# Performance work log

Hardware: AMD Instinct MI355X
Metric: run time of the kernel (lower is better)

The kernel has to match this reference:

```python
import jax, jax.numpy as jnp
import numpy as np

B, L, D_MODEL = 2, 2048, 1024
D_INNER, D_STATE, D_CONV, DT_RANK = 2048, 16, 4, 64  # expand=2, dt_rank=ceil(1024/16)


def setup_inputs() -> dict:
    key = jax.random.key(0)
    ks = jax.random.split(key, 12)
    s = lambda k, shape, sc=0.02: jax.random.normal(k, shape, dtype=jnp.float32) * sc
    return {
        "x": jax.random.normal(ks[0], (B, L, D_MODEL), dtype=jnp.float32),
        "norm_w": jnp.ones((D_MODEL,), jnp.float32),
        "norm_b": jnp.zeros((D_MODEL,), jnp.float32),
        "in_proj_w": s(ks[1], (2 * D_INNER, D_MODEL)),
        "conv_w": s(ks[2], (D_INNER, 1, D_CONV), 0.1),
        "conv_b": s(ks[3], (D_INNER,), 0.1),
        "x_proj_w": s(ks[4], (DT_RANK + 2 * D_STATE, D_INNER)),
        "dt_proj_w": s(ks[5], (D_INNER, DT_RANK), 0.1),
        "dt_proj_b": s(ks[6], (D_INNER,), 0.5),
        "A_log": jnp.log(jnp.broadcast_to(jnp.arange(1, D_STATE + 1, dtype=jnp.float32), (D_INNER, D_STATE))),
        "D": jnp.ones((D_INNER,), jnp.float32),
        "out_proj_w": s(ks[7], (D_MODEL, D_INNER)),
    }


def _layernorm(x, w, b, eps=1e-5):
    mu = jnp.mean(x, axis=-1, keepdims=True)
    var = jnp.var(x, axis=-1, keepdims=True)
    return (x - mu) * jax.lax.rsqrt(var + eps) * w + b


def _mamba_forward(x, norm_w, norm_b, in_proj_w, conv_w, conv_b, x_proj_w,
                   dt_proj_w, dt_proj_b, A_log, D, out_proj_w):
    residual = x
    xn = _layernorm(x, norm_w, norm_b)
    # in_proj -> split into x-branch and gate z
    xz = jnp.einsum('bld,ed->ble', xn, in_proj_w)  # [B,L,2*D_INNER]
    xc, z = jnp.split(xz, 2, axis=-1)
    # causal depthwise conv1d over time
    xt = jnp.transpose(xc, (0, 2, 1))  # [B,C,L]
    xt = jnp.pad(xt, ((0, 0), (0, 0), (D_CONV - 1, 0)))
    xt = jax.lax.conv_general_dilated(
        xt, conv_w, window_strides=(1,), padding=[(0, 0)],
        feature_group_count=D_INNER,
        dimension_numbers=('NCH', 'OIH', 'NCH')) + conv_b[None, :, None]
    u = jax.nn.silu(jnp.transpose(xt, (0, 2, 1)))  # [B,L,D_INNER]
    # input-dependent dt, B, C
    x_dbl = jnp.einsum('bld,ed->ble', u, x_proj_w)
    dt, Bm, Cm = jnp.split(x_dbl, [DT_RANK, DT_RANK + D_STATE], axis=-1)
    dt = jax.nn.softplus(jnp.einsum('blr,dr->bld', dt, dt_proj_w) + dt_proj_b)  # [B,L,D_INNER]
    A = -jnp.exp(A_log)  # [D_INNER, D_STATE]

    def step(h, inp):
        dt_t, B_t, C_t, u_t = inp  # [B,Di],[B,Ds],[B,Ds],[B,Di]
        dA = jnp.exp(dt_t[..., None] * A)                       # [B,Di,Ds]
        h = dA * h + (dt_t * u_t)[..., None] * B_t[:, None, :]  # [B,Di,Ds]
        y_t = jnp.einsum('bds,bs->bd', h, C_t)
        return h, y_t

    xs = (jnp.transpose(dt, (1, 0, 2)), jnp.transpose(Bm, (1, 0, 2)),
          jnp.transpose(Cm, (1, 0, 2)), jnp.transpose(u, (1, 0, 2)))
    h0 = jnp.zeros((B, D_INNER, D_STATE), dtype=x.dtype)
    _, ys = jax.lax.scan(step, h0, xs)
    y = jnp.transpose(ys, (1, 0, 2)) + u * D  # [B,L,D_INNER]
    y = y * jax.nn.silu(z)
    out = jnp.einsum('ble,de->bld', y, out_proj_w)
    # dropout in eval mode = identity
    return residual + out


def reference(x, norm_w, norm_b, in_proj_w, conv_w, conv_b, x_proj_w,
              dt_proj_w, dt_proj_b, A_log, D, out_proj_w):
    return _mamba_forward(x, norm_w, norm_b, in_proj_w, conv_w, conv_b, x_proj_w,
                          dt_proj_w, dt_proj_b, A_log, D, out_proj_w)
```

## Files before the change

### kernel.cpp

```cpp
#include <hip/hip_runtime.h>
#include <hip/hip_bf16.h>
#include <math.h>

#define BB 2
#define LL 2048
#define DMODEL 1024
#define DINNER 2048
#define DSTATE 16
#define DTRANK 64
#define NROWS (BB * LL)
#define NC 32
#define CK 64
#define KS 16
#define KCH (DINNER / KS)

typedef __bf16 bf16x8 __attribute__((ext_vector_type(8)));
typedef float  f32x4  __attribute__((ext_vector_type(4)));
typedef __attribute__((address_space(3))) void       as3_void;
typedef const __attribute__((address_space(1))) void as1_cvoid;

__device__ __forceinline__ ushort f2bf(float x) {
    __hip_bfloat16 h = __float2bfloat16(x);
    return *(ushort*)&h;
}

__global__ __launch_bounds__(256) void ln_kernel(const float* __restrict__ x,
                                                 const float* __restrict__ w,
                                                 const float* __restrict__ b,
                                                 __hip_bfloat16* __restrict__ xn) {
    int row = blockIdx.x;
    const float* xr = x + (size_t)row * DMODEL;
    float4 v = reinterpret_cast<const float4*>(xr)[threadIdx.x];
    float s  = v.x + v.y + v.z + v.w;
    float ss = v.x * v.x + v.y * v.y + v.z * v.z + v.w * v.w;
    for (int off = 32; off > 0; off >>= 1) {
        s  += __shfl_down(s, off);
        ss += __shfl_down(ss, off);
    }
    __shared__ float red0[4], red1[4];
    __shared__ float mu_s, rstd_s;
    int lane = threadIdx.x & 63, wv = threadIdx.x >> 6;
    if (lane == 0) { red0[wv] = s; red1[wv] = ss; }
    __syncthreads();
    if (threadIdx.x == 0) {
        float S = red0[0] + red0[1] + red0[2] + red0[3];
        float SS = red1[0] + red1[1] + red1[2] + red1[3];
        float mu = S * (1.0f / DMODEL);
        float var = SS * (1.0f / DMODEL) - mu * mu;
        mu_s = mu;
        rstd_s = rsqrtf(var + 1e-5f);
    }
    __syncthreads();
    float mu = mu_s, rstd = rstd_s;
    float4 wv4 = reinterpret_cast<const float4*>(w)[threadIdx.x];
    float4 bv4 = reinterpret_cast<const float4*>(b)[threadIdx.x];
    ushort4 o;
    o.x = f2bf((v.x - mu) * rstd * wv4.x + bv4.x);
    o.y = f2bf((v.y - mu) * rstd * wv4.y + bv4.y);
    o.z = f2bf((v.z - mu) * rstd * wv4.z + bv4.z);
    o.w = f2bf((v.w - mu) * rstd * wv4.w + bv4.w);
    *reinterpret_cast<ushort4*>((ushort*)xn + (size_t)row * DMODEL + threadIdx.x * 4) = o;
}

__global__ __launch_bounds__(256) void cvt_kernel(const float* __restrict__ in,
                                                  __hip_bfloat16* __restrict__ o) {
    int i = (blockIdx.x * 256 + threadIdx.x) * 4;
    float4 v = *reinterpret_cast<const float4*>(in + i);
    ushort4 p;
    p.x = f2bf(v.x); p.y = f2bf(v.y); p.z = f2bf(v.z); p.w = f2bf(v.w);
    *reinterpret_cast<ushort4*>((ushort*)o + i) = p;
}

template <int EPI>
__global__ __launch_bounds__(256) void gemm_bf16(
    const __hip_bfloat16* __restrict__ A, int lda,
    const __hip_bfloat16* __restrict__ W, int ldw,
    float* __restrict__ C, float* __restrict__ C2, int nsplit, int ldc,
    int K, const float* __restrict__ R) {
    __shared__ ushort As[128][32];
    __shared__ ushort Bs[128][32];
    int tid = threadIdx.x;
    int w = tid >> 6, lane = tid & 63;
    int m0 = blockIdx.y * 128, n0 = blockIdx.x * 128;
    int wr = w >> 1, wc = w & 1;

    int srow = (w << 4) + (lane >> 2);
    int skoff = (lane & 3) << 3;
    const ushort* gA = (const ushort*)A + (size_t)(m0 + srow) * lda + skoff;
    const ushort* gB = (const ushort*)W + (size_t)(n0 + srow) * ldw + skoff;
    char* ldsA0 = (char*)&As[0][0] + w * 1024;
    char* ldsB0 = (char*)&Bs[0][0] + w * 1024;

    f32x4 acc[4][4] = {};
    int frow = (lane & 15);
    int fk   = (lane >> 4) << 3;

    for (int k0 = 0; k0 < K; k0 += 32) {
        __syncthreads();
        __builtin_amdgcn_global_load_lds((as1_cvoid*)(gA + k0),                    (as3_void*)(ldsA0),        16, 0, 0);
        __builtin_amdgcn_global_load_lds((as1_cvoid*)(gA + (size_t)64 * lda + k0), (as3_void*)(ldsA0 + 4096), 16, 0, 0);
        __builtin_amdgcn_global_load_lds((as1_cvoid*)(gB + k0),                    (as3_void*)(ldsB0),        16, 0, 0);
        __builtin_amdgcn_global_load_lds((as1_cvoid*)(gB + (size_t)64 * ldw + k0), (as3_void*)(ldsB0 + 4096), 16, 0, 0);
        __syncthreads();

        bf16x8 af[4], bfr[4];
#pragma unroll
        for (int mi = 0; mi < 4; mi++)
            af[mi] = *(const bf16x8*)&As[wr * 64 + mi * 16 + frow][fk];
#pragma unroll
        for (int ni = 0; ni < 4; ni++)
            bfr[ni] = *(const bf16x8*)&Bs[wc * 64 + ni * 16 + frow][fk];
#pragma unroll
        for (int mi = 0; mi < 4; mi++)
#pragma unroll
            for (int ni = 0; ni < 4; ni++)
                acc[mi][ni] = __builtin_amdgcn_mfma_f32_16x16x32_bf16(
                    af[mi], bfr[ni], acc[mi][ni], 0, 0, 0);
    }

    int crow = (lane >> 4) << 2;
    int ccol = lane & 15;
    float* Cb = C;
    int nbase = n0;
    if (EPI == 0 && n0 >= nsplit) { Cb = C2; nbase = n0 - nsplit; }
#pragma unroll
    for (int mi = 0; mi < 4; mi++) {
#pragma unroll
        for (int ni = 0; ni < 4; ni++) {
#pragma unroll
            for (int r = 0; r < 4; r++) {
                int m = m0 + wr * 64 + mi * 16 + crow + r;
                int n = nbase + wc * 64 + ni * 16 + ccol;
                float v = acc[mi][ni][r];
                if (EPI == 2) v += R[(size_t)m * ldc + n];
                Cb[(size_t)m * ldc + n] = v;
            }
        }
    }
}

template <int EPI>
__global__ __launch_bounds__(256) void gemm_kernel(
    const float* __restrict__ A, int lda,
    const float* __restrict__ W, int ldw,
    float* __restrict__ C, int ldc,
    int N, int K,
    const float* __restrict__ bias) {
    __shared__ float As[16][64];
    __shared__ float Ws[16][64];
    int m0 = blockIdx.y * 64;
    int n0 = blockIdx.x * 64;
    int tid = threadIdx.x;
    int tm = tid >> 4, tn = tid & 15;
    int lr = tid >> 2;
    int lk = (tid & 3) << 2;

    float acc[4][4] = {};

    for (int k0 = 0; k0 < K; k0 += 16) {
        float4 av = *reinterpret_cast<const float4*>(A + (size_t)(m0 + lr) * lda + k0 + lk);
        float4 wvv;
        int wn = n0 + lr;
        if (wn < N)
            wvv = *reinterpret_cast<const float4*>(W + (size_t)wn * ldw + k0 + lk);
        else
            wvv = make_float4(0.f, 0.f, 0.f, 0.f);
        __syncthreads();
        As[lk + 0][lr] = av.x; As[lk + 1][lr] = av.y;
        As[lk + 2][lr] = av.z; As[lk + 3][lr] = av.w;
        Ws[lk + 0][lr] = wvv.x; Ws[lk + 1][lr] = wvv.y;
        Ws[lk + 2][lr] = wvv.z; Ws[lk + 3][lr] = wvv.w;
        __syncthreads();
#pragma unroll
        for (int k = 0; k < 16; k++) {
            float4 a = *reinterpret_cast<const float4*>(&As[k][tm << 2]);
            float4 bv = *reinterpret_cast<const float4*>(&Ws[k][tn << 2]);
            float ar[4] = {a.x, a.y, a.z, a.w};
            float br[4] = {bv.x, bv.y, bv.z, bv.w};
#pragma unroll
            for (int i = 0; i < 4; i++)
#pragma unroll
                for (int j = 0; j < 4; j++)
                    acc[i][j] = fmaf(ar[i], br[j], acc[i][j]);
        }
    }
#pragma unroll
    for (int i = 0; i < 4; i++) {
        int m = m0 + (tm << 2) + i;
#pragma unroll
        for (int j = 0; j < 4; j++) {
            int n = n0 + (tn << 2) + j;
            if (n < N) {
                float v = acc[i][j];
                if (EPI == 1) {
                    v += bias[n];
                    v = (v > 20.f) ? v : log1pf(__expf(v));
                }
                C[(size_t)m * ldc + n] = v;
            }
        }
    }
}

__global__ __launch_bounds__(256) void xp_partial(
    const float* __restrict__ A,
    const float* __restrict__ W,
    float* __restrict__ P) {
    __shared__ float As[16][64];
    __shared__ float Ws[16][64];
    int m0 = blockIdx.y * 64;
    int n0 = blockIdx.x * 64;
    int kbase = blockIdx.z * KCH;
    int tid = threadIdx.x;
    int tm = tid >> 4, tn = tid & 15;
    int lr = tid >> 2;
    int lk = (tid & 3) << 2;

    float acc[4][4] = {};

    for (int k0 = kbase; k0 < kbase + KCH; k0 += 16) {
        float4 av = *reinterpret_cast<const float4*>(A + (size_t)(m0 + lr) * DINNER + k0 + lk);
        float4 wvv;
        int wn = n0 + lr;
        if (wn < 96)
            wvv = *reinterpret_cast<const float4*>(W + (size_t)wn * DINNER + k0 + lk);
        else
            wvv = make_float4(0.f, 0.f, 0.f, 0.f);
        __syncthreads();
        As[lk + 0][lr] = av.x; As[lk + 1][lr] = av.y;
        As[lk + 2][lr] = av.z; As[lk + 3][lr] = av.w;
        Ws[lk + 0][lr] = wvv.x; Ws[lk + 1][lr] = wvv.y;
        Ws[lk + 2][lr] = wvv.z; Ws[lk + 3][lr] = wvv.w;
        __syncthreads();
#pragma unroll
        for (int k = 0; k < 16; k++) {
            float4 a = *reinterpret_cast<const float4*>(&As[k][tm << 2]);
            float4 bv = *reinterpret_cast<const float4*>(&Ws[k][tn << 2]);
            float ar[4] = {a.x, a.y, a.z, a.w};
            float br[4] = {bv.x, bv.y, bv.z, bv.w};
#pragma unroll
            for (int i = 0; i < 4; i++)
#pragma unroll
                for (int j = 0; j < 4; j++)
                    acc[i][j] = fmaf(ar[i], br[j], acc[i][j]);
        }
    }
    float* Pz = P + (size_t)blockIdx.z * NROWS * 96;
#pragma unroll
    for (int i = 0; i < 4; i++) {
        int m = m0 + (tm << 2) + i;
#pragma unroll
        for (int j = 0; j < 4; j++) {
            int n = n0 + (tn << 2) + j;
            if (n < 96)
                Pz[(size_t)m * 96 + n] = acc[i][j];
        }
    }
}

__global__ __launch_bounds__(256) void xp_reduce(
    const float* __restrict__ P, float* __restrict__ xdbl) {
    int i = blockIdx.x * 256 + threadIdx.x;
    float s = 0.f;
#pragma unroll
    for (int z = 0; z < KS; z++)
        s += P[(size_t)z * NROWS * 96 + i];
    xdbl[i] = s;
}

__global__ __launch_bounds__(256) void conv_silu_kernel(
    const float* __restrict__ xc, const float* __restrict__ cw,
    const float* __restrict__ cb, float* __restrict__ u) {
    int c = blockIdx.x * 256 + threadIdx.x;
    int r = blockIdx.y;
    int l = r & (LL - 1);
    float4 wv = reinterpret_cast<const float4*>(cw)[c];
    const float* p = xc + (size_t)r * DINNER + c;
    float acc = cb[c];
    if (l >= 3) acc = fmaf(p[-3 * DINNER], wv.x, acc);
    if (l >= 2) acc = fmaf(p[-2 * DINNER], wv.y, acc);
    if (l >= 1) acc = fmaf(p[-1 * DINNER], wv.z, acc);
    acc = fmaf(p[0], wv.w, acc);
    float sig = 1.f / (1.f + __expf(-acc));
    u[(size_t)r * DINNER + c] = acc * sig;
}

__global__ __launch_bounds__(256) void scan_pass1(
    const float* __restrict__ dt, const float* __restrict__ u,
    const float* __restrict__ xdbl, const float* __restrict__ A_log,
    float* __restrict__ hloc, float* __restrict__ aprod) {
    int bc = blockIdx.x >> 3;
    int b = bc >> 5, c = bc & (NC - 1);
    int d = ((blockIdx.x & 7) << 8) + threadIdx.x;
    float a2[DSTATE];
#pragma unroll
    for (int s = 0; s < DSTATE; s++)
        a2[s] = -__expf(A_log[d * DSTATE + s]) * 1.44269504089f;
    float h[DSTATE], ap[DSTATE];
#pragma unroll
    for (int s = 0; s < DSTATE; s++) { h[s] = 0.f; ap[s] = 1.f; }

    int t0 = c * CK;
    const float* dtp = dt + ((size_t)b * LL + t0) * DINNER + d;
    const float* up  = u  + ((size_t)b * LL + t0) * DINNER + d;
    const float* xr0 = xdbl + ((size_t)b * LL + t0) * 96;

    for (int t = 0; t < CK; t++) {
        float dtv = dtp[(size_t)t * DINNER];
        float uv  = up[(size_t)t * DINNER];
        float du  = dtv * uv;
        const float* xr = xr0 + t * 96;
#pragma unroll
        for (int s = 0; s < DSTATE; s++) {
            float dA = exp2f(dtv * a2[s]);
            h[s] = fmaf(dA, h[s], du * xr[64 + s]);
            ap[s] *= dA;
        }
    }
    size_t base = ((size_t)bc * DSTATE) * DINNER + d;
#pragma unroll
    for (int s = 0; s < DSTATE; s++) {
        hloc[base + (size_t)s * DINNER]  = h[s];
        aprod[base + (size_t)s * DINNER] = ap[s];
    }
}

__global__ __launch_bounds__(256) void scan_pass2(
    float* __restrict__ hloc, const float* __restrict__ aprod) {
    int idx = blockIdx.x * 256 + threadIdx.x;
    int d = idx & (DINNER - 1);
    int s = (idx >> 11) & (DSTATE - 1);
    int b = idx >> 15;
    float run = 0.f;
    for (int c = 0; c < NC; c++) {
        size_t off = ((size_t)((b * NC + c) * DSTATE + s)) * DINNER + d;
        float hl = hloc[off];
        float ap = aprod[off];
        hloc[off] = run;
        run = fmaf(ap, run, hl);
    }
}

__global__ __launch_bounds__(256) void scan_pass3(
    const float* __restrict__ dt, const float* __restrict__ u,
    const float* __restrict__ xdbl, const float* __restrict__ zb,
    const float* __restrict__ A_log, const float* __restrict__ Dp,
    const float* __restrict__ hinit, __hip_bfloat16* __restrict__ y) {
    int bc = blockIdx.x >> 3;
    int b = bc >> 5, c = bc & (NC - 1);
    int d = ((blockIdx.x & 7) << 8) + threadIdx.x;
    float a2[DSTATE];
#pragma unroll
    for (int s = 0; s < DSTATE; s++)
        a2[s] = -__expf(A_log[d * DSTATE + s]) * 1.44269504089f;
    float Dd = Dp[d];
    float h[DSTATE];
    size_t base = ((size_t)bc * DSTATE) * DINNER + d;
#pragma unroll
    for (int s = 0; s < DSTATE; s++) h[s] = hinit[base + (size_t)s * DINNER];

    int t0 = c * CK;
    const float* dtp = dt + ((size_t)b * LL + t0) * DINNER + d;
    const float* up  = u  + ((size_t)b * LL + t0) * DINNER + d;
    const float* zp  = zb + ((size_t)b * LL + t0) * DINNER + d;
    const float* xr0 = xdbl + ((size_t)b * LL + t0) * 96;
    ushort* yp = (ushort*)y + ((size_t)b * LL + t0) * DINNER + d;

    for (int t = 0; t < CK; t++) {
        float dtv = dtp[(size_t)t * DINNER];
        float uv  = up[(size_t)t * DINNER];
        float du  = dtv * uv;
        const float* xr = xr0 + t * 96;
        float yv = 0.f;
#pragma unroll
        for (int s = 0; s < DSTATE; s++) {
            float dA = exp2f(dtv * a2[s]);
            h[s] = fmaf(dA, h[s], du * xr[64 + s]);
            yv = fmaf(h[s], xr[80 + s], yv);
        }
        float zv = zp[(size_t)t * DINNER];
        float sig = 1.f / (1.f + __expf(-zv));
        yv = (yv + uv * Dd) * (zv * sig);
        yp[(size_t)t * DINNER] = f2bf(yv);
    }
}

extern "C" void kernel_launch(void* const* d_in, const int* in_sizes, int n_in,
                              void* d_out, int out_size, void* d_ws, size_t ws_size,
                              hipStream_t stream) {
    const float* x         = (const float*)d_in[0];
    const float* norm_w    = (const float*)d_in[1];
    const float* norm_b    = (const float*)d_in[2];
    const float* in_proj_w = (const float*)d_in[3];
    const float* conv_w    = (const float*)d_in[4];
    const float* conv_b    = (const float*)d_in[5];
    const float* x_proj_w  = (const float*)d_in[6];
    const float* dt_proj_w = (const float*)d_in[7];
    const float* dt_proj_b = (const float*)d_in[8];
    const float* A_log     = (const float*)d_in[9];
    const float* Dp        = (const float*)d_in[10];
    const float* out_proj_w= (const float*)d_in[11];
    float* out = (float*)d_out;

    float* ws   = (float*)d_ws;
    const size_t NI = (size_t)NROWS * DINNER;
    float* xc   = ws;
    float* zb   = xc + NI;
    float* u    = zb + NI;
    float* dtb  = u + NI;
    float* xdbl = dtb + NI;
    __hip_bfloat16* xnb = (__hip_bfloat16*)(xdbl + (size_t)NROWS * 96);
    __hip_bfloat16* ybb = xnb + (size_t)NROWS * DMODEL;
    __hip_bfloat16* wib = ybb + NI;
    __hip_bfloat16* wob = wib + (size_t)2 * DINNER * DMODEL;
    float* hloc  = xc;
    float* aprod = xc + (size_t)BB * NC * DSTATE * DINNER;
    float* xpp   = dtb;

    ln_kernel<<<NROWS, 256, 0, stream>>>(x, norm_w, norm_b, xnb);
    cvt_kernel<<<(2 * DINNER * DMODEL) / 1024, 256, 0, stream>>>(in_proj_w, wib);
    cvt_kernel<<<(DMODEL * DINNER) / 1024, 256, 0, stream>>>(out_proj_w, wob);
    gemm_bf16<0><<<dim3((2 * DINNER) / 128, NROWS / 128), 256, 0, stream>>>(
        xnb, DMODEL, wib, DMODEL, xc, zb, DINNER, DINNER, DMODEL, nullptr);
    conv_silu_kernel<<<dim3(DINNER / 256, NROWS), 256, 0, stream>>>(xc, conv_w, conv_b, u);
    xp_partial<<<dim3(2, NROWS / 64, KS), 256, 0, stream>>>(u, x_proj_w, xpp);
    xp_reduce<<<(NROWS * 96) / 256, 256, 0, stream>>>(xpp, xdbl);
    gemm_kernel<1><<<dim3(DINNER / 64, NROWS / 64), 256, 0, stream>>>(
        xdbl, 96, dt_proj_w, DTRANK, dtb, DINNER, DINNER, DTRANK, dt_proj_b);
    scan_pass1<<<BB * NC * (DINNER / 256), 256, 0, stream>>>(dtb, u, xdbl, A_log, hloc, aprod);
    scan_pass2<<<(BB * DSTATE * DINNER) / 256, 256, 0, stream>>>(hloc, aprod);
    scan_pass3<<<BB * NC * (DINNER / 256), 256, 0, stream>>>(dtb, u, xdbl, zb, A_log, Dp, hloc, ybb);
    gemm_bf16<2><<<dim3(DMODEL / 128, NROWS / 128), 256, 0, stream>>>(
        ybb, DINNER, wob, DINNER, out, nullptr, 1 << 30, DMODEL, DINNER, x);
}
```

Before: 430.4 us.

## Store z, dt and scan copy of u in bf16; halve scan chunk length

The in_proj epilogue now writes the gate z in bf16, the dt_proj epilogue writes dt in bf16, and conv_silu writes a bf16 copy of u alongside the fp32 one. The scan passes read these half-width arrays, which cuts the memory traffic of the bandwidth-bound scan kernels. The scan chunking also changes from 32 chunks of 64 steps to 64 chunks of 32, which doubles the blocks per pass for more parallelism but lengthens the serial prefix in pass 2 and doubles the size of the hloc/aprod buffers. Keeping dt and u in bf16 adds rounding error to the recurrence.

```diff
diff --git a/kernel.cpp b/kernel.cpp
--- a/kernel.cpp
+++ b/kernel.cpp
@@ -9,8 +9,8 @@
 #define DSTATE 16
 #define DTRANK 64
 #define NROWS (BB * LL)
-#define NC 32
-#define CK 64
+#define NC 64
+#define CK 32
 #define KS 16
 #define KCH (DINNER / KS)
 
@@ -22,6 +22,10 @@
 __device__ __forceinline__ ushort f2bf(float x) {
     __hip_bfloat16 h = __float2bfloat16(x);
     return *(ushort*)&h;
+}
+__device__ __forceinline__ float bf2f(ushort u) {
+    unsigned int v = ((unsigned int)u) << 16;
+    return *(float*)&v;
 }
 
 __global__ __launch_bounds__(256) void ln_kernel(const float* __restrict__ x,
@@ -120,9 +124,8 @@
 
     int crow = (lane >> 4) << 2;
     int ccol = lane & 15;
-    float* Cb = C;
-    int nbase = n0;
-    if (EPI == 0 && n0 >= nsplit) { Cb = C2; nbase = n0 - nsplit; }
+    bool toz = (EPI == 0) && (n0 >= nsplit);
+    int nbase = toz ? (n0 - nsplit) : n0;
 #pragma unroll
     for (int mi = 0; mi < 4; mi++) {
 #pragma unroll
@@ -133,7 +136,10 @@
                 int n = nbase + wc * 64 + ni * 16 + ccol;
                 float v = acc[mi][ni][r];
                 if (EPI == 2) v += R[(size_t)m * ldc + n];
-                Cb[(size_t)m * ldc + n] = v;
+                if (toz)
+                    ((ushort*)C2)[(size_t)m * ldc + n] = f2bf(v);
+                else
+                    C[(size_t)m * ldc + n] = v;
             }
         }
     }
@@ -195,8 +201,10 @@
                 if (EPI == 1) {
                     v += bias[n];
                     v = (v > 20.f) ? v : log1pf(__expf(v));
+                    ((ushort*)C)[(size_t)m * ldc + n] = f2bf(v);
+                } else {
+                    C[(size_t)m * ldc + n] = v;
                 }
-                C[(size_t)m * ldc + n] = v;
             }
         }
     }
@@ -270,7 +278,8 @@
 
 __global__ __launch_bounds__(256) void conv_silu_kernel(
     const float* __restrict__ xc, const float* __restrict__ cw,
-    const float* __restrict__ cb, float* __restrict__ u) {
+    const float* __restrict__ cb, float* __restrict__ u32,
+    ushort* __restrict__ u16) {
     int c = blockIdx.x * 256 + threadIdx.x;
     int r = blockIdx.y;
     int l = r & (LL - 1);
@@ -282,15 +291,17 @@
     if (l >= 1) acc = fmaf(p[-1 * DINNER], wv.z, acc);
     acc = fmaf(p[0], wv.w, acc);
     float sig = 1.f / (1.f + __expf(-acc));
-    u[(size_t)r * DINNER + c] = acc * sig;
+    float uv = acc * sig;
+    u32[(size_t)r * DINNER + c] = uv;
+    u16[(size_t)r * DINNER + c] = f2bf(uv);
 }
 
 __global__ __launch_bounds__(256) void scan_pass1(
-    const float* __restrict__ dt, const float* __restrict__ u,
+    const ushort* __restrict__ dt16, const ushort* __restrict__ u16,
     const float* __restrict__ xdbl, const float* __restrict__ A_log,
     float* __restrict__ hloc, float* __restrict__ aprod) {
     int bc = blockIdx.x >> 3;
-    int b = bc >> 5, c = bc & (NC - 1);
+    int b = bc >> 6, c = bc & (NC - 1);
     int d = ((blockIdx.x & 7) << 8) + threadIdx.x;
     float a2[DSTATE];
 #pragma unroll
@@ -301,13 +312,13 @@
     for (int s = 0; s < DSTATE; s++) { h[s] = 0.f; ap[s] = 1.f; }
 
     int t0 = c * CK;
-    const float* dtp = dt + ((size_t)b * LL + t0) * DINNER + d;
-    const float* up  = u  + ((size_t)b * LL + t0) * DINNER + d;
-    const float* xr0 = xdbl + ((size_t)b * LL + t0) * 96;
+    const ushort* dtp = dt16 + ((size_t)b * LL + t0) * DINNER + d;
+    const ushort* up  = u16  + ((size_t)b * LL + t0) * DINNER + d;
+    const float* xr0  = xdbl + ((size_t)b * LL + t0) * 96;
 
     for (int t = 0; t < CK; t++) {
-        float dtv = dtp[(size_t)t * DINNER];
-        float uv  = up[(size_t)t * DINNER];
+        float dtv = bf2f(dtp[(size_t)t * DINNER]);
+        float uv  = bf2f(up[(size_t)t * DINNER]);
         float du  = dtv * uv;
         const float* xr = xr0 + t * 96;
 #pragma unroll
@@ -342,12 +353,12 @@
 }
 
 __global__ __launch_bounds__(256) void scan_pass3(
-    const float* __restrict__ dt, const float* __restrict__ u,
-    const float* __restrict__ xdbl, const float* __restrict__ zb,
+    const ushort* __restrict__ dt16, const ushort* __restrict__ u16,
+    const float* __restrict__ xdbl, const ushort* __restrict__ zb,
     const float* __restrict__ A_log, const float* __restrict__ Dp,
     const float* __restrict__ hinit, __hip_bfloat16* __restrict__ y) {
     int bc = blockIdx.x >> 3;
-    int b = bc >> 5, c = bc & (NC - 1);
+    int b = bc >> 6, c = bc & (NC - 1);
     int d = ((blockIdx.x & 7) << 8) + threadIdx.x;
     float a2[DSTATE];
 #pragma unroll
@@ -360,15 +371,15 @@
     for (int s = 0; s < DSTATE; s++) h[s] = hinit[base + (size_t)s * DINNER];
 
     int t0 = c * CK;
-    const float* dtp = dt + ((size_t)b * LL + t0) * DINNER + d;
-    const float* up  = u  + ((size_t)b * LL + t0) * DINNER + d;
-    const float* zp  = zb + ((size_t)b * LL + t0) * DINNER + d;
-    const float* xr0 = xdbl + ((size_t)b * LL + t0) * 96;
+    const ushort* dtp = dt16 + ((size_t)b * LL + t0) * DINNER + d;
+    const ushort* up  = u16  + ((size_t)b * LL + t0) * DINNER + d;
+    const ushort* zp  = zb   + ((size_t)b * LL + t0) * DINNER + d;
+    const float* xr0  = xdbl + ((size_t)b * LL + t0) * 96;
     ushort* yp = (ushort*)y + ((size_t)b * LL + t0) * DINNER + d;
 
     for (int t = 0; t < CK; t++) {
-        float dtv = dtp[(size_t)t * DINNER];
-        float uv  = up[(size_t)t * DINNER];
+        float dtv = bf2f(dtp[(size_t)t * DINNER]);
+        float uv  = bf2f(up[(size_t)t * DINNER]);
         float du  = dtv * uv;
         const float* xr = xr0 + t * 96;
         float yv = 0.f;
@@ -378,7 +389,7 @@
             h[s] = fmaf(dA, h[s], du * xr[64 + s]);
             yv = fmaf(h[s], xr[80 + s], yv);
         }
-        float zv = zp[(size_t)t * DINNER];
+        float zv = bf2f(zp[(size_t)t * DINNER]);
         float sig = 1.f / (1.f + __expf(-zv));
         yv = (yv + uv * Dd) * (zv * sig);
         yp[(size_t)t * DINNER] = f2bf(yv);
@@ -404,32 +415,37 @@
 
     float* ws   = (float*)d_ws;
     const size_t NI = (size_t)NROWS * DINNER;
-    float* xc   = ws;
-    float* zb   = xc + NI;
-    float* u    = zb + NI;
-    float* dtb  = u + NI;
-    float* xdbl = dtb + NI;
+    float* xc    = ws;
+    float* zbF   = xc + NI;
+    ushort* zb   = (ushort*)zbF;
+    float* u32   = zbF + NI / 2;
+    ushort* u16  = (ushort*)(u32 + NI);
+    ushort* dt16 = (ushort*)(u32 + NI + NI / 2);
+    float* xdbl  = u32 + NI + NI / 2 + NI / 2;
     __hip_bfloat16* xnb = (__hip_bfloat16*)(xdbl + (size_t)NROWS * 96);
     __hip_bfloat16* ybb = xnb + (size_t)NROWS * DMODEL;
     __hip_bfloat16* wib = ybb + NI;
     __hip_bfloat16* wob = wib + (size_t)2 * DINNER * DMODEL;
     float* hloc  = xc;
     float* aprod = xc + (size_t)BB * NC * DSTATE * DINNER;
-    float* xpp   = dtb;
+    float* xpp   = xc;
 
     ln_kernel<<<NROWS, 256, 0, stream>>>(x, norm_w, norm_b, xnb);
     cvt_kernel<<<(2 * DINNER * DMODEL) / 1024, 256, 0, stream>>>(in_proj_w, wib);
     cvt_kernel<<<(DMODEL * DINNER) / 1024, 256, 0, stream>>>(out_proj_w, wob);
     gemm_bf16<0><<<dim3((2 * DINNER) / 128, NROWS / 128), 256, 0, stream>>>(
-        xnb, DMODEL, wib, DMODEL, xc, zb, DINNER, DINNER, DMODEL, nullptr);
-    conv_silu_kernel<<<dim3(DINNER / 256, NROWS), 256, 0, stream>>>(xc, conv_w, conv_b, u);
-    xp_partial<<<dim3(2, NROWS / 64, KS), 256, 0, stream>>>(u, x_proj_w, xpp);
+        xnb, DMODEL, wib, DMODEL, xc, zbF, DINNER, DINNER, DMODEL, nullptr);
+    conv_silu_kernel<<<dim3(DINNER / 256, NROWS), 256, 0, stream>>>(
+        xc, conv_w, conv_b, u32, u16);
+    xp_partial<<<dim3(2, NROWS / 64, KS), 256, 0, stream>>>(u32, x_proj_w, xpp);
     xp_reduce<<<(NROWS * 96) / 256, 256, 0, stream>>>(xpp, xdbl);
     gemm_kernel<1><<<dim3(DINNER / 64, NROWS / 64), 256, 0, stream>>>(
-        xdbl, 96, dt_proj_w, DTRANK, dtb, DINNER, DINNER, DTRANK, dt_proj_b);
-    scan_pass1<<<BB * NC * (DINNER / 256), 256, 0, stream>>>(dtb, u, xdbl, A_log, hloc, aprod);
+        xdbl, 96, dt_proj_w, DTRANK, (float*)dt16, DINNER, DINNER, DTRANK, dt_proj_b);
+    scan_pass1<<<BB * NC * (DINNER / 256), 256, 0, stream>>>(
+        dt16, u16, xdbl, A_log, hloc, aprod);
     scan_pass2<<<(BB * DSTATE * DINNER) / 256, 256, 0, stream>>>(hloc, aprod);
-    scan_pass3<<<BB * NC * (DINNER / 256), 256, 0, stream>>>(dtb, u, xdbl, zb, A_log, Dp, hloc, ybb);
+    scan_pass3<<<BB * NC * (DINNER / 256), 256, 0, stream>>>(
+        dt16, u16, xdbl, zb, A_log, Dp, hloc, ybb);
     gemm_bf16<2><<<dim3(DMODEL / 128, NROWS / 128), 256, 0, stream>>>(
         ybb, DINNER, wob, DINNER, out, nullptr, 1 << 30, DMODEL, DINNER, x);
 }
```

Result: no change. 425.5 us (-1.1%).
